# Optimization experiments

Measured on AMD Instinct MI355X. Metric: run time of the kernel, lower is better.

Reference implementation:

```python
import jax, jax.numpy as jnp
import numpy as np

B, N, HIST, PRED, KHOP, H = 64, 1085, 24, 24, 3, 64
FX, FM = 1, 11
F = FX + FM  # node feature dim fed to gnn (12)
E = 17360


def setup_inputs() -> dict:
    key = jax.random.key(0)
    ks = jax.random.split(key, 13)
    s = 0.1
    return {
        "x_hist": jax.random.normal(ks[0], (B, HIST, N, FX), jnp.float32),
        "enc_misc": jax.random.normal(ks[1], (B, HIST, N, FM), jnp.float32),
        "dec": jax.random.normal(ks[2], (B, PRED, N, FM), jnp.float32),
        "We": jax.random.normal(ks[3], (2 * F, F), jnp.float32) * s,
        "be": jnp.zeros((F,), jnp.float32),
        "Wx": jax.random.normal(ks[4], (KHOP, 2 * F, 3 * H), jnp.float32) * s,
        "Wh": jax.random.normal(ks[5], (KHOP, H, 3 * H), jnp.float32) * s,
        "bx": jnp.zeros((KHOP, 3 * H), jnp.float32),
        "bh": jnp.zeros((KHOP, 3 * H), jnp.float32),
        "fc_w": jax.random.normal(ks[6], (KHOP * H, FX), jnp.float32) * s,
        "fc_b": jnp.zeros((FX,), jnp.float32),
        "src": jax.random.randint(ks[7], (E,), 0, N, jnp.int32),
        "dst": jax.random.randint(ks[8], (E,), 0, N, jnp.int32),
    }


def reference(x_hist, enc_misc, dec, We, be, Wx, Wh, bx, bh, fc_w, fc_b, src, dst):
    features = jnp.concatenate([enc_misc, dec], axis=1)  # (B, HIST+PRED, N, FM)

    def gnn(x):  # x: (B, N, F) -> (B, N, F); edge MLP + scatter-sum + residual
        m = jax.nn.relu(jnp.concatenate([x[:, src], x[:, dst]], -1) @ We + be)  # (B,E,F)
        return x + jnp.zeros_like(x).at[:, dst].add(m)

    def gru(x, h, k):  # x: (B*N, 2F), h: (B*N, H)
        g = x @ Wx[k] + bx[k]
        gh = h @ Wh[k] + bh[k]
        r = jax.nn.sigmoid(g[:, :H] + gh[:, :H])
        z = jax.nn.sigmoid(g[:, H:2 * H] + gh[:, H:2 * H])
        n = jnp.tanh(g[:, 2 * H:] + r * gh[:, 2 * H:])
        return (1.0 - z) * n + z * h

    def run_step(hn, xn):  # xn: (B, N, F)
        xg = xn
        new = list(hn)
        for k in range(KHOP):
            xg = gnn(xg)
            x_gru = jnp.concatenate([xg, xn], -1).reshape(B * N, 2 * F)
            new[k] = gru(x_gru, new[k], k)
        return tuple(new)

    h0 = tuple(jnp.zeros((B * N, H), x_hist.dtype) for _ in range(KHOP))

    def hist_step(hn, inp):
        xp, ft = inp  # (B,N,FX), (B,N,FM)
        return run_step(hn, jnp.concatenate([xp, ft], -1)), None

    hist_xs = (jnp.swapaxes(x_hist[:, :HIST - 1], 0, 1),
               jnp.swapaxes(features[:, 1:HIST], 0, 1))
    hn, _ = jax.lax.scan(hist_step, h0, hist_xs)

    def pred_step(carry, ft):
        hn, x = carry
        hn = run_step(hn, jnp.concatenate([x, ft], -1))
        hn_all = jnp.concatenate([h.reshape(B, N, H) for h in hn], -1)  # (B,N,KHOP*H)
        x_new = hn_all @ fc_w + fc_b  # (B, N, FX)
        return (hn, x_new), x_new

    _, ys = jax.lax.scan(pred_step, (hn, x_hist[:, -1]),
                         jnp.swapaxes(features[:, HIST:], 0, 1))
    return jnp.swapaxes(ys, 0, 1)  # (B, PRED, N, FX)
```

## Files before the change

kernel.cpp:

```cpp
#include <hip/hip_runtime.h>

#define NB 64
#define NNODE 1085
#define HIST 24
#define PRED 24
#define KHOP 3
#define HDIM 64
#define FXD 1
#define FMD 11
#define FD 12
#define NE 17360
#define NROWS (NB*NNODE)
#define WPAR 1024


typedef float v4 __attribute__((ext_vector_type(4)));

__device__ __forceinline__ float sigm(float x){ return 1.0f/(1.0f + __expf(-x)); }
__device__ __forceinline__ float tanh_f(float x){ return 1.0f - 2.0f/(__expf(2.0f*x)+1.0f); }

__global__ void csr_count_k(const int* __restrict__ dst, int* __restrict__ deg)
{
    int e = blockIdx.x*256 + threadIdx.x;
    if (e < NE) atomicAdd(&deg[dst[e]], 1);
}

__global__ __launch_bounds__(1024) void csr_scan_k(const int* __restrict__ deg,
                                                   int* __restrict__ offs, int* __restrict__ curs)
{
    __shared__ int s[2][2048];
    int t = threadIdx.x;
    for (int i=t;i<2048;i+=1024) s[0][i] = (i<NNODE) ? deg[i] : 0;
    __syncthreads();
    int cur = 0;
    for (int d=1; d<2048; d<<=1){
        for (int i=t;i<2048;i+=1024){
            int v = s[cur][i];
            if (i>=d) v += s[cur][i-d];
            s[cur^1][i] = v;
        }
        __syncthreads();
        cur ^= 1;
    }
    for (int i=t;i<=NNODE;i+=1024){
        int v = (i==0) ? 0 : s[cur][i-1];
        offs[i] = v;
        if (i<NNODE) curs[i] = v;
    }
}

__global__ void csr_fill_k(const int* __restrict__ dst, const int* __restrict__ src,
                           int* __restrict__ curs, int* __restrict__ esrc)
{
    int e = blockIdx.x*256 + threadIdx.x;
    if (e < NE){
        int d = dst[e];
        int p = atomicAdd(&curs[d], 1);
        esrc[p] = src[e];
    }
}

__global__ void csr_part_k(const int* __restrict__ offs, int* __restrict__ wpart)
{
    int w = blockIdx.x*256 + threadIdx.x;
    if (w > WPAR) return;
    if (w == 0)    { wpart[0] = 0;        return; }
    if (w == WPAR) { wpart[WPAR] = NNODE; return; }
    int target = (int)(((long)w * NE) / WPAR);
    int lo = 0, hi = NNODE;
    while (lo < hi){ int mid = (lo+hi)>>1; if (offs[mid] >= target) hi = mid; else lo = mid+1; }
    wpart[w] = lo;
}

__global__ void build_hist_k(const float* __restrict__ x_hist, const float* __restrict__ enc_misc,
                             int t0, int T, float* __restrict__ xn_all)
{
    long idx = (long)blockIdx.x*256 + threadIdx.x;
    if (idx >= (long)T*NROWS) return;
    int b = (int)(idx & 63);
    long nn = idx >> 6;
    int ti = (int)(nn / NNODE);
    int n  = (int)(nn - (long)ti*NNODE);
    int t  = t0 + ti;
    float* xp = xn_all + (long)ti*NROWS*FD + (long)n*FD*64 + b;
    xp[0] = x_hist[((long)b*HIST + t)*NNODE + n];
    const float* fp = enc_misc + (((long)b*HIST + (t+1))*NNODE + n)*FMD;
    #pragma unroll
    for (int i=0;i<FMD;i++) xp[(1+i)*64] = fp[i];
}

__global__ void build_xn_k(const float* __restrict__ xsrc, int from_xcur,
                           const float* __restrict__ dec, int p,
                           float* __restrict__ xn)
{
    int idx = blockIdx.x*256 + threadIdx.x;
    if (idx >= NROWS) return;
    int b = idx & 63, n = idx >> 6;
    float v0 = from_xcur ? xsrc[idx]
                         : xsrc[((long)b*HIST + (HIST-1))*NNODE + n];
    float* xp = xn + (long)n*FD*64 + b;
    xp[0] = v0;
    const float* fp = dec + (((long)b*PRED + p)*NNODE + n)*FMD;
    #pragma unroll
    for (int i=0;i<FMD;i++) xp[(1+i)*64] = fp[i];
}

__global__ __launch_bounds__(256) void gnn_gather_k(const float* __restrict__ xin,
    const float* __restrict__ We, const float* __restrict__ be,
    const int* __restrict__ esrc, const int* __restrict__ offs,
    const int* __restrict__ wpart, float* __restrict__ xout)
{
    __shared__ float w_s[288];
    __shared__ float be_s[12];
    const int tid = threadIdx.x;
    for (int i=tid;i<288;i+=256) w_s[i]=We[i];
    if (tid<12) be_s[tid]=be[tid];
    __syncthreads();

    const int lane = tid & 63;
    const int wave = (blockIdx.x*256 + tid) >> 6;
    const long sbase = (long)blockIdx.y * ((long)NROWS*FD);
    const float* x = xin + sbase;
    float* xo = xout + sbase;

    const int n0 = wpart[wave], n1 = wpart[wave+1];
    for (int n=n0; n<n1; ++n){
        float xd[12], part[12], acc[12];
        const float* xb = x + (long)n*768 + lane;
        #pragma unroll
        for (int f=0;f<12;f++) xd[f] = xb[f*64];
        #pragma unroll
        for (int f=0;f<12;f++){ part[f]=be_s[f]; acc[f]=0.f; }
        #pragma unroll
        for (int f=0;f<12;f++){
            float xv = xd[f];
            const float* wrow = &w_s[(12+f)*12];
            #pragma unroll
            for (int j=0;j<12;j++) part[j] += xv*wrow[j];
        }
        const int e0 = offs[n], e1 = offs[n+1];
        for (int idx=e0; idx<e1; ++idx){
            int s = esrc[idx];
            const float* xsb = x + (long)s*768 + lane;
            float m[12];
            #pragma unroll
            for (int f=0;f<12;f++) m[f]=part[f];
            #pragma unroll
            for (int f=0;f<12;f++){
                float xv = xsb[f*64];
                const float* wrow = &w_s[f*12];
                #pragma unroll
                for (int j=0;j<12;j++) m[j] += xv*wrow[j];
            }
            #pragma unroll
            for (int f=0;f<12;f++) acc[f] += fmaxf(m[f],0.f);
        }
        float* xob = xo + (long)n*768 + lane;
        #pragma unroll
        for (int f=0;f<12;f++) xob[f*64] = xd[f] + acc[f];
    }
}

#define KC 44
__global__ __launch_bounds__(256) void gru3_k(
    const float* __restrict__ xg_base, long k_stride,
    const float* __restrict__ xn,
    float* __restrict__ h_base,
    const float* __restrict__ Wx, const float* __restrict__ Wh,
    const float* __restrict__ bx, const float* __restrict__ bh)
{
    const int k = blockIdx.y;
    const int n = blockIdx.x;
    const float* xgn = xg_base + (long)k*k_stride + (long)n*768;
    const float* xnn = xn + (long)n*768;
    float*       hn  = h_base + ((size_t)k*NROWS + (long)n*64)*HDIM;
    const float* wx  = Wx + (size_t)k*24*192;
    const float* wh  = Wh + (size_t)k*64*192;
    const float* bxk = bx + k*192;
    const float* bhk = bh + k*192;

    __shared__ __align__(16) float A_s[KC][64];
    __shared__ __align__(16) float W_s[KC][192];
    const int tid = threadIdx.x;
    const int tx = tid & 15, ty = tid >> 4;

    const v4* wx4 = (const v4*)wx;
    const v4* wh4 = (const v4*)wh;
    const v4* h4  = (const v4*)hn;

    float acc_r[16], acc_z[16], acc_gn[16], acc_ghn[16];
    #pragma unroll
    for (int i=0;i<16;i++){ acc_r[i]=0.f; acc_z[i]=0.f; acc_gn[i]=0.f; acc_ghn[i]=0.f; }

    for (int i=tid; i<KC*48; i+=256){
        int kk = i/48, q = i - kk*48;
        v4 w = (kk<24) ? wx4[kk*48+q] : wh4[(kk-24)*48+q];
        *(v4*)&W_s[kk][q*4] = w;
    }
    for (int i=tid; i<192; i+=256) ((v4*)A_s)[i]       = ((const v4*)xgn)[i];
    for (int i=tid; i<192; i+=256) ((v4*)A_s)[192+i]   = ((const v4*)xnn)[i];
    for (int i=tid; i<320; i+=256){
        int r = i/5, q = i - r*5;
        v4 v = h4[r*16+q];
        #pragma unroll
        for (int j=0;j<4;j++) A_s[24+4*q+j][r] = v[j];
    }
    __syncthreads();
    #pragma unroll 4
    for (int kk=0;kk<24;kk++){
        v4 av=*(const v4*)&A_s[kk][ty*4];
        v4 wr=*(const v4*)&W_s[kk][tx*4];
        v4 wz=*(const v4*)&W_s[kk][64+tx*4];
        v4 wn=*(const v4*)&W_s[kk][128+tx*4];
        #pragma unroll
        for (int dr=0;dr<4;dr++)
            #pragma unroll
            for (int dc=0;dc<4;dc++){
                acc_r[dr*4+dc]+=av[dr]*wr[dc];
                acc_z[dr*4+dc]+=av[dr]*wz[dc];
                acc_gn[dr*4+dc]+=av[dr]*wn[dc];
            }
    }
    #pragma unroll 4
    for (int kk=24;kk<44;kk++){
        v4 av=*(const v4*)&A_s[kk][ty*4];
        v4 wr=*(const v4*)&W_s[kk][tx*4];
        v4 wz=*(const v4*)&W_s[kk][64+tx*4];
        v4 wn=*(const v4*)&W_s[kk][128+tx*4];
        #pragma unroll
        for (int dr=0;dr<4;dr++)
            #pragma unroll
            for (int dc=0;dc<4;dc++){
                acc_r[dr*4+dc]+=av[dr]*wr[dc];
                acc_z[dr*4+dc]+=av[dr]*wz[dc];
                acc_ghn[dr*4+dc]+=av[dr]*wn[dc];
            }
    }
    __syncthreads();
    for (int i=tid; i<KC*48; i+=256){
        int kk = i/48, q = i - kk*48;
        *(v4*)&W_s[kk][q*4] = wh4[(20+kk)*48+q];
    }
    for (int i=tid; i<704; i+=256){
        int r = i/11, q = i - r*11;
        v4 v = h4[r*16+5+q];
        #pragma unroll
        for (int j=0;j<4;j++) A_s[4*q+j][r] = v[j];
    }
    __syncthreads();
    #pragma unroll 4
    for (int kk=0;kk<44;kk++){
        v4 av=*(const v4*)&A_s[kk][ty*4];
        v4 wr=*(const v4*)&W_s[kk][tx*4];
        v4 wz=*(const v4*)&W_s[kk][64+tx*4];
        v4 wn=*(const v4*)&W_s[kk][128+tx*4];
        #pragma unroll
        for (int dr=0;dr<4;dr++)
            #pragma unroll
            for (int dc=0;dc<4;dc++){
                acc_r[dr*4+dc]+=av[dr]*wr[dc];
                acc_z[dr*4+dc]+=av[dr]*wz[dc];
                acc_ghn[dr*4+dc]+=av[dr]*wn[dc];
            }
    }

    v4 bxr=*(const v4*)&bxk[tx*4],     bhr=*(const v4*)&bhk[tx*4];
    v4 bxz=*(const v4*)&bxk[64+tx*4],  bhz=*(const v4*)&bhk[64+tx*4];
    v4 bxn=*(const v4*)&bxk[128+tx*4], bhn=*(const v4*)&bhk[128+tx*4];
    #pragma unroll
    for (int dr=0;dr<4;dr++){
        int lr = ty*4 + dr;
        v4 hold = *(const v4*)&hn[lr*HDIM + tx*4];
        v4 hnew;
        #pragma unroll
        for (int dc=0;dc<4;dc++){
            float rr = sigm(acc_r[dr*4+dc] + bxr[dc] + bhr[dc]);
            float zz = sigm(acc_z[dr*4+dc] + bxz[dc] + bhz[dc]);
            float nn = tanh_f(acc_gn[dr*4+dc] + bxn[dc] + rr*(acc_ghn[dr*4+dc] + bhn[dc]));
            hnew[dc] = (1.0f-zz)*nn + zz*hold[dc];
        }
        *(v4*)&hn[lr*HDIM + tx*4] = hnew;
    }
}

__global__ void fc_k(const float* __restrict__ h, const float* __restrict__ fc_w,
                     const float* __restrict__ fc_b, float* __restrict__ x_cur,
                     float* __restrict__ out, int p)
{
    int idx = blockIdx.x*256+threadIdx.x;
    if (idx>=NROWS) return;
    float acc = fc_b[0];
    #pragma unroll
    for (int k=0;k<3;k++){
        const float* hb = h + ((size_t)k*NROWS + idx)*HDIM;
        const float* wb = fc_w + k*HDIM;
        #pragma unroll
        for (int q=0;q<16;q++){
            v4 hv=*(const v4*)&hb[q*4];
            v4 wv=*(const v4*)&wb[q*4];
            acc += hv[0]*wv[0]+hv[1]*wv[1]+hv[2]*wv[2]+hv[3]*wv[3];
        }
    }
    x_cur[idx]=acc;
    int b = idx & 63, n = idx >> 6;
    out[((long)b*PRED + p)*NNODE + n] = acc;
}

extern "C" void kernel_launch(void* const* d_in, const int* in_sizes, int n_in,
                              void* d_out, int out_size, void* d_ws, size_t ws_size,
                              hipStream_t stream)
{
    const float* x_hist   = (const float*)d_in[0];
    const float* enc_misc = (const float*)d_in[1];
    const float* dec      = (const float*)d_in[2];
    const float* We       = (const float*)d_in[3];
    const float* be       = (const float*)d_in[4];
    const float* Wx       = (const float*)d_in[5];
    const float* Wh       = (const float*)d_in[6];
    const float* bx       = (const float*)d_in[7];
    const float* bh       = (const float*)d_in[8];
    const float* fc_w     = (const float*)d_in[9];
    const float* fc_b     = (const float*)d_in[10];
    const int*   src      = (const int*)d_in[11];
    const int*   dst      = (const int*)d_in[12];
    float* out = (float*)d_out;

    const size_t SZ_T = (size_t)NROWS*FD;
    size_t fixed_f = (size_t)3*NROWS*HDIM + NROWS + 64*1024;
    size_t avail_f = ws_size/4;
    long tc = 1;
    if (avail_f > fixed_f + 4*SZ_T)
        tc = (long)((avail_f - fixed_f) / (4*SZ_T));
    if (tc > HIST-1) tc = HIST-1;
    if (tc < 1) tc = 1;
    const long T_CHUNK = tc;

    float* h      = (float*)d_ws;
    float* x_cur  = h + (size_t)3*NROWS*HDIM;
    int*   deg    = (int*)(x_cur + NROWS);
    int*   offs   = deg + NNODE;
    int*   curs   = offs + NNODE + 1;
    int*   wpart  = curs + NNODE;
    int*   esrc   = wpart + WPAR + 1;
    float* xn_all = (float*)(esrc + NE) + 16;
    xn_all = (float*)(((size_t)xn_all + 255) & ~(size_t)255);
    float* xg_all = xn_all + T_CHUNK*SZ_T;
    const long K_STRIDE = T_CHUNK*SZ_T;

    hipMemsetAsync(h, 0, (size_t)3*NROWS*HDIM*sizeof(float), stream);
    hipMemsetAsync(deg, 0, NNODE*sizeof(int), stream);

    const int gE = (NE+255)/256;
    csr_count_k<<<gE,256,0,stream>>>(dst, deg);
    csr_scan_k<<<1,1024,0,stream>>>(deg, offs, curs);
    csr_fill_k<<<gE,256,0,stream>>>(dst, src, curs, esrc);
    csr_part_k<<<(WPAR+256)/256,256,0,stream>>>(offs, wpart);

    const int gRow = (NROWS+255)/256;
    const int gGx  = WPAR*64/256;

    for (int t0 = 0; t0 < HIST-1; t0 += (int)T_CHUNK){
        int T = min((int)T_CHUNK, HIST-1-t0);
        build_hist_k<<<(int)(((long)T*NROWS+255)/256),256,0,stream>>>(x_hist, enc_misc, t0, T, xn_all);
        dim3 gG(gGx, T);
        gnn_gather_k<<<gG,256,0,stream>>>(xn_all,            We,be,esrc,offs,wpart, xg_all);
        gnn_gather_k<<<gG,256,0,stream>>>(xg_all,            We,be,esrc,offs,wpart, xg_all+K_STRIDE);
        gnn_gather_k<<<gG,256,0,stream>>>(xg_all+K_STRIDE,   We,be,esrc,offs,wpart, xg_all+2*K_STRIDE);
        for (int ti=0; ti<T; ti++){
            dim3 gU(NNODE, 3);
            gru3_k<<<gU,256,0,stream>>>(xg_all + ti*SZ_T, K_STRIDE,
                                        xn_all + ti*SZ_T, h, Wx, Wh, bx, bh);
        }
    }

    for (int p=0;p<PRED;p++){
        if (p==0)
            build_xn_k<<<gRow,256,0,stream>>>(x_hist, 0, dec, p, xn_all);
        else
            build_xn_k<<<gRow,256,0,stream>>>(x_cur, 1, dec, p, xn_all);
        dim3 gG(gGx, 1);
        gnn_gather_k<<<gG,256,0,stream>>>(xn_all,          We,be,esrc,offs,wpart, xg_all);
        gnn_gather_k<<<gG,256,0,stream>>>(xg_all,          We,be,esrc,offs,wpart, xg_all+K_STRIDE);
        gnn_gather_k<<<gG,256,0,stream>>>(xg_all+K_STRIDE, We,be,esrc,offs,wpart, xg_all+2*K_STRIDE);
        dim3 gU(NNODE, 3);
        gru3_k<<<gU,256,0,stream>>>(xg_all, K_STRIDE, xn_all, h, Wx, Wh, bx, bh);
        fc_k<<<gRow,256,0,stream>>>(h, fc_w, fc_b, x_cur, out, p);
    }
}
```

Measured before the change: 13.63 ms.

## Run GRU matmuls on bf16 MFMA with split hi/lo precision and finer pred partitions

New measurement: 24.92 ms. 82.8% more time.

```diff
diff --git a/kernel.cpp b/kernel.cpp
--- a/kernel.cpp
+++ b/kernel.cpp
@@ -4,20 +4,30 @@
 #define NNODE 1085
 #define HIST 24
 #define PRED 24
-#define KHOP 3
 #define HDIM 64
-#define FXD 1
 #define FMD 11
 #define FD 12
 #define NE 17360
 #define NROWS (NB*NNODE)
-#define WPAR 1024
+#define WPARH 1024
+#define WPARP 8192
+#define SZT ((long)NROWS*FD)
 
 
 typedef float v4 __attribute__((ext_vector_type(4)));
+typedef float f32x4 __attribute__((ext_vector_type(4)));
+typedef short short8 __attribute__((ext_vector_type(8)));
 
 __device__ __forceinline__ float sigm(float x){ return 1.0f/(1.0f + __expf(-x)); }
 __device__ __forceinline__ float tanh_f(float x){ return 1.0f - 2.0f/(__expf(2.0f*x)+1.0f); }
+__device__ __forceinline__ unsigned short f2bf(float f){
+    union { float f; unsigned u; } v; v.f = f;
+    unsigned r = v.u + 0x7FFF + ((v.u >> 16) & 1);
+    return (unsigned short)(r >> 16);
+}
+__device__ __forceinline__ float bf2f(unsigned short u){
+    union { unsigned u; float f; } v; v.u = ((unsigned)u)<<16; return v.f;
+}
 
 __global__ void csr_count_k(const int* __restrict__ dst, int* __restrict__ deg)
 {
@@ -60,16 +70,44 @@
     }
 }
 
-__global__ void csr_part_k(const int* __restrict__ offs, int* __restrict__ wpart)
+__global__ void csr_part_k(const int* __restrict__ offs, int* __restrict__ wpart, int npart)
 {
     int w = blockIdx.x*256 + threadIdx.x;
-    if (w > WPAR) return;
-    if (w == 0)    { wpart[0] = 0;        return; }
-    if (w == WPAR) { wpart[WPAR] = NNODE; return; }
-    int target = (int)(((long)w * NE) / WPAR);
+    if (w > npart) return;
+    if (w == 0)     { wpart[0] = 0;         return; }
+    if (w == npart) { wpart[npart] = NNODE; return; }
+    int target = (int)(((long)w * NE) / npart);
     int lo = 0, hi = NNODE;
     while (lo < hi){ int mid = (lo+hi)>>1; if (offs[mid] >= target) hi = mid; else lo = mid+1; }
     wpart[w] = lo;
+}
+
+__global__ void prep_k(const float* __restrict__ Wx, const float* __restrict__ Wh,
+                       const float* __restrict__ bx, const float* __restrict__ bh,
+                       unsigned short* __restrict__ Wt, float* __restrict__ bpack)
+{
+    int id = blockIdx.x*256 + threadIdx.x;
+    if (id < 3*192*192){
+        int hop = id/(192*192); int rem = id - hop*192*192;
+        int n = rem/192, kk = rem - n*192;
+        int k2 = (kk < 96) ? kk : kk - 96;
+        float v = 0.f;
+        if (k2 < 24)       v = Wx[hop*24*192 + k2*192 + n];
+        else if (k2 >= 32) v = Wh[hop*64*192 + (k2-32)*192 + n];
+        unsigned short hi = f2bf(v);
+        Wt[id] = (kk < 96) ? hi : f2bf(v - bf2f(hi));
+    }
+    if (id < 3*4*64){
+        int hop = id/256; int rem = id - hop*256;
+        int g = rem>>6, c = rem&63;
+        const float* bxk = bx + hop*192; const float* bhk = bh + hop*192;
+        float v;
+        if (g==0)      v = bxk[c]     + bhk[c];
+        else if (g==1) v = bxk[64+c]  + bhk[64+c];
+        else if (g==2) v = bxk[128+c];
+        else           v = bhk[128+c];
+        bpack[id] = v;
+    }
 }
 
 __global__ void build_hist_k(const float* __restrict__ x_hist, const float* __restrict__ enc_misc,
@@ -82,7 +120,7 @@
     int ti = (int)(nn / NNODE);
     int n  = (int)(nn - (long)ti*NNODE);
     int t  = t0 + ti;
-    float* xp = xn_all + (long)ti*NROWS*FD + (long)n*FD*64 + b;
+    float* xp = xn_all + (long)ti*SZT + (long)n*FD*64 + b;
     xp[0] = x_hist[((long)b*HIST + t)*NNODE + n];
     const float* fp = enc_misc + (((long)b*HIST + (t+1))*NNODE + n)*FMD;
     #pragma unroll
@@ -96,8 +134,7 @@
     int idx = blockIdx.x*256 + threadIdx.x;
     if (idx >= NROWS) return;
     int b = idx & 63, n = idx >> 6;
-    float v0 = from_xcur ? xsrc[idx]
-                         : xsrc[((long)b*HIST + (HIST-1))*NNODE + n];
+    float v0 = from_xcur ? xsrc[idx] : xsrc[((long)b*HIST + (HIST-1))*NNODE + n];
     float* xp = xn + (long)n*FD*64 + b;
     xp[0] = v0;
     const float* fp = dec + (((long)b*PRED + p)*NNODE + n)*FMD;
@@ -105,7 +142,7 @@
     for (int i=0;i<FMD;i++) xp[(1+i)*64] = fp[i];
 }
 
-__global__ __launch_bounds__(256) void gnn_gather_k(const float* __restrict__ xin,
+__global__ __launch_bounds__(256,4) void gnn_gather_k(const float* __restrict__ xin,
     const float* __restrict__ We, const float* __restrict__ be,
     const int* __restrict__ esrc, const int* __restrict__ offs,
     const int* __restrict__ wpart, float* __restrict__ xout)
@@ -119,9 +156,9 @@
 
     const int lane = tid & 63;
     const int wave = (blockIdx.x*256 + tid) >> 6;
-    const long sbase = (long)blockIdx.y * ((long)NROWS*FD);
-    const float* x = xin + sbase;
-    float* xo = xout + sbase;
+    const long ti = blockIdx.y;
+    const float* x = xin + ti*SZT;
+    float* xo = xout + ti*SZT;
 
     const int n0 = wpart[wave], n1 = wpart[wave+1];
     for (int n=n0; n<n1; ++n){
@@ -140,8 +177,8 @@
         }
         const int e0 = offs[n], e1 = offs[n+1];
         for (int idx=e0; idx<e1; ++idx){
-            int s = esrc[idx];
-            const float* xsb = x + (long)s*768 + lane;
+            int s2 = esrc[idx];
+            const float* xsb = x + (long)s2*768 + lane;
             float m[12];
             #pragma unroll
             for (int f=0;f<12;f++) m[f]=part[f];
@@ -161,129 +198,117 @@
     }
 }
 
-#define KC 44
-__global__ __launch_bounds__(256) void gru3_k(
+__global__ __launch_bounds__(256,2) void gru_mfma_k(
     const float* __restrict__ xg_base, long k_stride,
     const float* __restrict__ xn,
-    float* __restrict__ h_base,
-    const float* __restrict__ Wx, const float* __restrict__ Wh,
-    const float* __restrict__ bx, const float* __restrict__ bh)
-{
-    const int k = blockIdx.y;
-    const int n = blockIdx.x;
-    const float* xgn = xg_base + (long)k*k_stride + (long)n*768;
-    const float* xnn = xn + (long)n*768;
-    float*       hn  = h_base + ((size_t)k*NROWS + (long)n*64)*HDIM;
-    const float* wx  = Wx + (size_t)k*24*192;
-    const float* wh  = Wh + (size_t)k*64*192;
-    const float* bxk = bx + k*192;
-    const float* bhk = bh + k*192;
-
-    __shared__ __align__(16) float A_s[KC][64];
-    __shared__ __align__(16) float W_s[KC][192];
+    const unsigned short* __restrict__ Wt,
+    const float* __restrict__ bpack,
+    unsigned short* __restrict__ hbf)
+{
+    __shared__ __align__(16) unsigned short Wt_s[192][200];
     const int tid = threadIdx.x;
-    const int tx = tid & 15, ty = tid >> 4;
-
-    const v4* wx4 = (const v4*)wx;
-    const v4* wh4 = (const v4*)wh;
-    const v4* h4  = (const v4*)hn;
-
-    float acc_r[16], acc_z[16], acc_gn[16], acc_ghn[16];
-    #pragma unroll
-    for (int i=0;i<16;i++){ acc_r[i]=0.f; acc_z[i]=0.f; acc_gn[i]=0.f; acc_ghn[i]=0.f; }
-
-    for (int i=tid; i<KC*48; i+=256){
-        int kk = i/48, q = i - kk*48;
-        v4 w = (kk<24) ? wx4[kk*48+q] : wh4[(kk-24)*48+q];
-        *(v4*)&W_s[kk][q*4] = w;
-    }
-    for (int i=tid; i<192; i+=256) ((v4*)A_s)[i]       = ((const v4*)xgn)[i];
-    for (int i=tid; i<192; i+=256) ((v4*)A_s)[192+i]   = ((const v4*)xnn)[i];
-    for (int i=tid; i<320; i+=256){
-        int r = i/5, q = i - r*5;
-        v4 v = h4[r*16+q];
-        #pragma unroll
-        for (int j=0;j<4;j++) A_s[24+4*q+j][r] = v[j];
+    const int n = blockIdx.x, hop = blockIdx.y;
+
+    const unsigned short* wtg = Wt + (size_t)hop*192*192;
+    #pragma unroll
+    for (int it=0; it<18; ++it){
+        int i = tid + it*256;
+        int r = i/24, o = i - r*24;
+        *(short8*)&Wt_s[r][o*8] = *(const short8*)&wtg[r*192 + o*8];
     }
     __syncthreads();
-    #pragma unroll 4
-    for (int kk=0;kk<24;kk++){
-        v4 av=*(const v4*)&A_s[kk][ty*4];
-        v4 wr=*(const v4*)&W_s[kk][tx*4];
-        v4 wz=*(const v4*)&W_s[kk][64+tx*4];
-        v4 wn=*(const v4*)&W_s[kk][128+tx*4];
-        #pragma unroll
-        for (int dr=0;dr<4;dr++)
-            #pragma unroll
-            for (int dc=0;dc<4;dc++){
-                acc_r[dr*4+dc]+=av[dr]*wr[dc];
-                acc_z[dr*4+dc]+=av[dr]*wz[dc];
-                acc_gn[dr*4+dc]+=av[dr]*wn[dc];
-            }
-    }
-    #pragma unroll 4
-    for (int kk=24;kk<44;kk++){
-        v4 av=*(const v4*)&A_s[kk][ty*4];
-        v4 wr=*(const v4*)&W_s[kk][tx*4];
-        v4 wz=*(const v4*)&W_s[kk][64+tx*4];
-        v4 wn=*(const v4*)&W_s[kk][128+tx*4];
-        #pragma unroll
-        for (int dr=0;dr<4;dr++)
-            #pragma unroll
-            for (int dc=0;dc<4;dc++){
-                acc_r[dr*4+dc]+=av[dr]*wr[dc];
-                acc_z[dr*4+dc]+=av[dr]*wz[dc];
-                acc_ghn[dr*4+dc]+=av[dr]*wn[dc];
-            }
-    }
-    __syncthreads();
-    for (int i=tid; i<KC*48; i+=256){
-        int kk = i/48, q = i - kk*48;
-        *(v4*)&W_s[kk][q*4] = wh4[(20+kk)*48+q];
-    }
-    for (int i=tid; i<704; i+=256){
-        int r = i/11, q = i - r*11;
-        v4 v = h4[r*16+5+q];
-        #pragma unroll
-        for (int j=0;j<4;j++) A_s[4*q+j][r] = v[j];
-    }
-    __syncthreads();
-    #pragma unroll 4
-    for (int kk=0;kk<44;kk++){
-        v4 av=*(const v4*)&A_s[kk][ty*4];
-        v4 wr=*(const v4*)&W_s[kk][tx*4];
-        v4 wz=*(const v4*)&W_s[kk][64+tx*4];
-        v4 wn=*(const v4*)&W_s[kk][128+tx*4];
-        #pragma unroll
-        for (int dr=0;dr<4;dr++)
-            #pragma unroll
-            for (int dc=0;dc<4;dc++){
-                acc_r[dr*4+dc]+=av[dr]*wr[dc];
-                acc_z[dr*4+dc]+=av[dr]*wz[dc];
-                acc_ghn[dr*4+dc]+=av[dr]*wn[dc];
-            }
-    }
-
-    v4 bxr=*(const v4*)&bxk[tx*4],     bhr=*(const v4*)&bhk[tx*4];
-    v4 bxz=*(const v4*)&bxk[64+tx*4],  bhz=*(const v4*)&bhk[64+tx*4];
-    v4 bxn=*(const v4*)&bxk[128+tx*4], bhn=*(const v4*)&bhk[128+tx*4];
-    #pragma unroll
-    for (int dr=0;dr<4;dr++){
-        int lr = ty*4 + dr;
-        v4 hold = *(const v4*)&hn[lr*HDIM + tx*4];
-        v4 hnew;
-        #pragma unroll
-        for (int dc=0;dc<4;dc++){
-            float rr = sigm(acc_r[dr*4+dc] + bxr[dc] + bhr[dc]);
-            float zz = sigm(acc_z[dr*4+dc] + bxz[dc] + bhz[dc]);
-            float nn = tanh_f(acc_gn[dr*4+dc] + bxn[dc] + rr*(acc_ghn[dr*4+dc] + bhn[dc]));
-            hnew[dc] = (1.0f-zz)*nn + zz*hold[dc];
-        }
-        *(v4*)&hn[lr*HDIM + tx*4] = hnew;
-    }
-}
-
-__global__ void fc_k(const float* __restrict__ h, const float* __restrict__ fc_w,
+
+    const int w = tid>>6, l = tid&63, lr = l&15, lk = l>>4;
+    const int b = w*16 + lr;
+    const long rowA = (long)n*64 + b;
+
+    short8 a0hi = short8(0), a0lo = short8(0);
+    if (lk < 3){
+        const float* xgn = xg_base + (long)hop*k_stride + (long)n*768 + b;
+        const float* xnn = xn + (long)n*768 + b;
+        #pragma unroll
+        for (int i=0;i<8;i++){
+            int k = lk*8 + i;
+            float v = (k<12) ? xgn[k*64] : xnn[(k-12)*64];
+            unsigned short hi = f2bf(v);
+            a0hi[i] = (short)hi;
+            a0lo[i] = (short)f2bf(v - bf2f(hi));
+        }
+    }
+    const unsigned short* hb = hbf + ((long)hop*NROWS + rowA)*128;
+    short8 a1hi = *(const short8*)&hb[lk*8];
+    short8 a2hi = *(const short8*)&hb[32 + lk*8];
+    short8 a1lo = *(const short8*)&hb[64 + lk*8];
+    short8 a2lo = *(const short8*)&hb[96 + lk*8];
+
+    f32x4 accRZ[8], accNX[4], accNH[4];
+    #pragma unroll
+    for (int i=0;i<8;i++) accRZ[i] = f32x4(0.f);
+    #pragma unroll
+    for (int i=0;i<4;i++){ accNX[i] = f32x4(0.f); accNH[i] = f32x4(0.f); }
+
+    #pragma unroll
+    for (int nt=0; nt<12; ++nt){
+        const unsigned short* wc = &Wt_s[nt*16 + lr][0];
+        short8 b0h = *(const short8*)&wc[lk*8];
+        short8 b1h = *(const short8*)&wc[32 + lk*8];
+        short8 b2h = *(const short8*)&wc[64 + lk*8];
+        short8 b0l = *(const short8*)&wc[96 + lk*8];
+        short8 b1l = *(const short8*)&wc[128 + lk*8];
+        short8 b2l = *(const short8*)&wc[160 + lk*8];
+        if (nt < 8){
+            f32x4 acc = accRZ[nt];
+            acc = __builtin_amdgcn_mfma_f32_16x16x32_bf16(a0hi, b0h, acc, 0,0,0);
+            acc = __builtin_amdgcn_mfma_f32_16x16x32_bf16(a0lo, b0h, acc, 0,0,0);
+            acc = __builtin_amdgcn_mfma_f32_16x16x32_bf16(a0hi, b0l, acc, 0,0,0);
+            acc = __builtin_amdgcn_mfma_f32_16x16x32_bf16(a1hi, b1h, acc, 0,0,0);
+            acc = __builtin_amdgcn_mfma_f32_16x16x32_bf16(a1lo, b1h, acc, 0,0,0);
+            acc = __builtin_amdgcn_mfma_f32_16x16x32_bf16(a1hi, b1l, acc, 0,0,0);
+            acc = __builtin_amdgcn_mfma_f32_16x16x32_bf16(a2hi, b2h, acc, 0,0,0);
+            acc = __builtin_amdgcn_mfma_f32_16x16x32_bf16(a2lo, b2h, acc, 0,0,0);
+            acc = __builtin_amdgcn_mfma_f32_16x16x32_bf16(a2hi, b2l, acc, 0,0,0);
+            accRZ[nt] = acc;
+        } else {
+            f32x4 ax = accNX[nt-8], ah = accNH[nt-8];
+            ax = __builtin_amdgcn_mfma_f32_16x16x32_bf16(a0hi, b0h, ax, 0,0,0);
+            ax = __builtin_amdgcn_mfma_f32_16x16x32_bf16(a0lo, b0h, ax, 0,0,0);
+            ax = __builtin_amdgcn_mfma_f32_16x16x32_bf16(a0hi, b0l, ax, 0,0,0);
+            ah = __builtin_amdgcn_mfma_f32_16x16x32_bf16(a1hi, b1h, ah, 0,0,0);
+            ah = __builtin_amdgcn_mfma_f32_16x16x32_bf16(a1lo, b1h, ah, 0,0,0);
+            ah = __builtin_amdgcn_mfma_f32_16x16x32_bf16(a1hi, b1l, ah, 0,0,0);
+            ah = __builtin_amdgcn_mfma_f32_16x16x32_bf16(a2hi, b2h, ah, 0,0,0);
+            ah = __builtin_amdgcn_mfma_f32_16x16x32_bf16(a2lo, b2h, ah, 0,0,0);
+            ah = __builtin_amdgcn_mfma_f32_16x16x32_bf16(a2hi, b2l, ah, 0,0,0);
+            accNX[nt-8] = ax; accNH[nt-8] = ah;
+        }
+    }
+
+    const float* bp = bpack + hop*256;
+    unsigned short* hbo = hbf + ((long)hop*NROWS + (long)n*64)*128;
+    #pragma unroll
+    for (int nt0=0; nt0<4; ++nt0){
+        int hcol = nt0*16 + lr;
+        float br  = bp[hcol];
+        float bz  = bp[64 + hcol];
+        float bxn = bp[128 + hcol];
+        float bhn = bp[192 + hcol];
+        #pragma unroll
+        for (int i=0;i<4;i++){
+            int orow = w*16 + lk*4 + i;
+            long off = (long)orow*128 + hcol;
+            float hold = bf2f(hbo[off]) + bf2f(hbo[off+64]);
+            float r  = sigm(accRZ[nt0][i] + br);
+            float z  = sigm(accRZ[4+nt0][i] + bz);
+            float nn2 = tanh_f(accNX[nt0][i] + bxn + r*(accNH[nt0][i] + bhn));
+            float hv = (1.f - z)*nn2 + z*hold;
+            unsigned short hvh = f2bf(hv);
+            hbo[off] = hvh;
+            hbo[off+64] = f2bf(hv - bf2f(hvh));
+        }
+    }
+}
+
+__global__ void fc_k(const unsigned short* __restrict__ hbf, const float* __restrict__ fc_w,
                      const float* __restrict__ fc_b, float* __restrict__ x_cur,
                      float* __restrict__ out, int p)
 {
@@ -292,13 +317,15 @@
     float acc = fc_b[0];
     #pragma unroll
     for (int k=0;k<3;k++){
-        const float* hb = h + ((size_t)k*NROWS + idx)*HDIM;
+        const unsigned short* hb = hbf + ((size_t)k*NROWS + idx)*128;
         const float* wb = fc_w + k*HDIM;
         #pragma unroll
-        for (int q=0;q<16;q++){
-            v4 hv=*(const v4*)&hb[q*4];
-            v4 wv=*(const v4*)&wb[q*4];
-            acc += hv[0]*wv[0]+hv[1]*wv[1]+hv[2]*wv[2]+hv[3]*wv[3];
+        for (int q=0;q<8;q++){
+            short8 hi8 = *(const short8*)&hb[q*8];
+            short8 lo8 = *(const short8*)&hb[64 + q*8];
+            #pragma unroll
+            for (int j=0;j<8;j++)
+                acc += (bf2f((unsigned short)hi8[j]) + bf2f((unsigned short)lo8[j])) * wb[q*8+j];
         }
     }
     x_cur[idx]=acc;
@@ -325,65 +352,72 @@
     const int*   dst      = (const int*)d_in[12];
     float* out = (float*)d_out;
 
-    const size_t SZ_T = (size_t)NROWS*FD;
-    size_t fixed_f = (size_t)3*NROWS*HDIM + NROWS + 64*1024;
-    size_t avail_f = ws_size/4;
-    long tc = 1;
-    if (avail_f > fixed_f + 4*SZ_T)
-        tc = (long)((avail_f - fixed_f) / (4*SZ_T));
-    if (tc > HIST-1) tc = HIST-1;
-    if (tc < 1) tc = 1;
-    const long T_CHUNK = tc;
-
-    float* h      = (float*)d_ws;
-    float* x_cur  = h + (size_t)3*NROWS*HDIM;
-    int*   deg    = (int*)(x_cur + NROWS);
-    int*   offs   = deg + NNODE;
-    int*   curs   = offs + NNODE + 1;
-    int*   wpart  = curs + NNODE;
-    int*   esrc   = wpart + WPAR + 1;
-    float* xn_all = (float*)(esrc + NE) + 16;
-    xn_all = (float*)(((size_t)xn_all + 255) & ~(size_t)255);
-    float* xg_all = xn_all + T_CHUNK*SZ_T;
-    const long K_STRIDE = T_CHUNK*SZ_T;
-
-    hipMemsetAsync(h, 0, (size_t)3*NROWS*HDIM*sizeof(float), stream);
-    hipMemsetAsync(deg, 0, NNODE*sizeof(int), stream);
+    char* p = (char*)d_ws;
+    auto alloc = [&](size_t bytes) -> char* {
+        p = (char*)(((size_t)p + 255) & ~(size_t)255);
+        char* r = p; p += bytes; return r;
+    };
+    unsigned short* hbf = (unsigned short*)alloc((size_t)3*NROWS*128*2);
+    unsigned short* Wt  = (unsigned short*)alloc((size_t)3*192*192*2);
+    float* bpack = (float*)alloc(3*4*64*4);
+    float* x_cur = (float*)alloc((size_t)NROWS*4);
+    int* deg    = (int*)alloc(NNODE*4);
+    int* offs   = (int*)alloc((NNODE+1)*4);
+    int* curs   = (int*)alloc(NNODE*4);
+    int* wpartH = (int*)alloc((WPARH+1)*4);
+    int* wpartP = (int*)alloc((WPARP+1)*4);
+    int* esrc   = (int*)alloc(NE*4);
+
+    const size_t perslice = (size_t)SZT*4*4;
+    size_t fixed_used = (size_t)(p - (char*)d_ws) + 8192;
+    long T_CHUNK = 1;
+    if (ws_size > fixed_used + perslice)
+        T_CHUNK = (long)((ws_size - fixed_used) / perslice);
+    if (T_CHUNK > HIST-1) T_CHUNK = HIST-1;
+    if (T_CHUNK < 1) T_CHUNK = 1;
+
+    float* xn_all = (float*)alloc((size_t)T_CHUNK*SZT*4);
+    float* xg_all = (float*)alloc((size_t)3*T_CHUNK*SZT*4);
+    const long K_STRIDE = T_CHUNK*SZT;
+
+    hipMemsetAsync(hbf, 0, (size_t)3*NROWS*128*2, stream);
+    hipMemsetAsync(deg, 0, NNODE*4, stream);
 
     const int gE = (NE+255)/256;
     csr_count_k<<<gE,256,0,stream>>>(dst, deg);
     csr_scan_k<<<1,1024,0,stream>>>(deg, offs, curs);
     csr_fill_k<<<gE,256,0,stream>>>(dst, src, curs, esrc);
-    csr_part_k<<<(WPAR+256)/256,256,0,stream>>>(offs, wpart);
+    csr_part_k<<<(WPARH+256)/256,256,0,stream>>>(offs, wpartH, WPARH);
+    csr_part_k<<<(WPARP+256)/256,256,0,stream>>>(offs, wpartP, WPARP);
+    prep_k<<<(3*192*192+255)/256,256,0,stream>>>(Wx, Wh, bx, bh, Wt, bpack);
 
     const int gRow = (NROWS+255)/256;
-    const int gGx  = WPAR*64/256;
 
     for (int t0 = 0; t0 < HIST-1; t0 += (int)T_CHUNK){
         int T = min((int)T_CHUNK, HIST-1-t0);
         build_hist_k<<<(int)(((long)T*NROWS+255)/256),256,0,stream>>>(x_hist, enc_misc, t0, T, xn_all);
-        dim3 gG(gGx, T);
-        gnn_gather_k<<<gG,256,0,stream>>>(xn_all,            We,be,esrc,offs,wpart, xg_all);
-        gnn_gather_k<<<gG,256,0,stream>>>(xg_all,            We,be,esrc,offs,wpart, xg_all+K_STRIDE);
-        gnn_gather_k<<<gG,256,0,stream>>>(xg_all+K_STRIDE,   We,be,esrc,offs,wpart, xg_all+2*K_STRIDE);
+        dim3 gH(WPARH/4, T);
+        gnn_gather_k<<<gH,256,0,stream>>>(xn_all,             We,be,esrc,offs,wpartH, xg_all);
+        gnn_gather_k<<<gH,256,0,stream>>>(xg_all,             We,be,esrc,offs,wpartH, xg_all+K_STRIDE);
+        gnn_gather_k<<<gH,256,0,stream>>>(xg_all+K_STRIDE,    We,be,esrc,offs,wpartH, xg_all+2*K_STRIDE);
         for (int ti=0; ti<T; ti++){
             dim3 gU(NNODE, 3);
-            gru3_k<<<gU,256,0,stream>>>(xg_all + ti*SZ_T, K_STRIDE,
-                                        xn_all + ti*SZ_T, h, Wx, Wh, bx, bh);
-        }
-    }
-
-    for (int p=0;p<PRED;p++){
-        if (p==0)
-            build_xn_k<<<gRow,256,0,stream>>>(x_hist, 0, dec, p, xn_all);
+            gru_mfma_k<<<gU,256,0,stream>>>(xg_all + ti*SZT, K_STRIDE,
+                                            xn_all + ti*SZT, Wt, bpack, hbf);
+        }
+    }
+
+    for (int pstep=0; pstep<PRED; pstep++){
+        if (pstep==0)
+            build_xn_k<<<gRow,256,0,stream>>>(x_hist, 0, dec, pstep, xn_all);
         else
-            build_xn_k<<<gRow,256,0,stream>>>(x_cur, 1, dec, p, xn_all);
-        dim3 gG(gGx, 1);
-        gnn_gather_k<<<gG,256,0,stream>>>(xn_all,          We,be,esrc,offs,wpart, xg_all);
-        gnn_gather_k<<<gG,256,0,stream>>>(xg_all,          We,be,esrc,offs,wpart, xg_all+K_STRIDE);
-        gnn_gather_k<<<gG,256,0,stream>>>(xg_all+K_STRIDE, We,be,esrc,offs,wpart, xg_all+2*K_STRIDE);
+            build_xn_k<<<gRow,256,0,stream>>>(x_cur, 1, dec, pstep, xn_all);
+        dim3 gP(WPARP/4, 1);
+        gnn_gather_k<<<gP,256,0,stream>>>(xn_all,          We,be,esrc,offs,wpartP, xg_all);
+        gnn_gather_k<<<gP,256,0,stream>>>(xg_all,          We,be,esrc,offs,wpartP, xg_all+K_STRIDE);
+        gnn_gather_k<<<gP,256,0,stream>>>(xg_all+K_STRIDE, We,be,esrc,offs,wpartP, xg_all+2*K_STRIDE);
         dim3 gU(NNODE, 3);
-        gru3_k<<<gU,256,0,stream>>>(xg_all, K_STRIDE, xn_all, h, Wx, Wh, bx, bh);
-        fc_k<<<gRow,256,0,stream>>>(h, fc_w, fc_b, x_cur, out, p);
-    }
-}
+        gru_mfma_k<<<gU,256,0,stream>>>(xg_all, K_STRIDE, xn_all, Wt, bpack, hbf);
+        fc_k<<<gRow,256,0,stream>>>(hbf, fc_w, fc_b, x_cur, out, pstep);
+    }
+}
```
